# Kernel tuning notes

Hardware: AMD Instinct MI355X
Metric: run time of the kernel (lower is better)

## Reference

```python
import jax, jax.numpy as jnp
import numpy as np

NUM_HEADS = 8


def setup_inputs() -> dict:
    key = jax.random.key(0)
    ks = jax.random.split(key, 9)
    B, S, E = 16, 2048, 768
    s = 0.02
    return {
        "features": jax.random.normal(ks[0], (B, S, E), jnp.float32),
        "in_proj_w": jax.random.normal(ks[1], (3 * E, E), jnp.float32) * s,
        "in_proj_b": jnp.zeros((3 * E,), jnp.float32),
        "out_proj_w": jax.random.normal(ks[2], (E, E), jnp.float32) * s,
        "out_proj_b": jnp.zeros((E,), jnp.float32),
        "w1": jax.random.normal(ks[3], (384, E), jnp.float32) * s,
        "b1": jnp.zeros((384,), jnp.float32),
        "w2": jax.random.normal(ks[4], (1, 384), jnp.float32) * s,
        "b2": jnp.zeros((1,), jnp.float32),
    }


def reference(features, in_proj_w, in_proj_b, out_proj_w, out_proj_b, w1, b1, w2, b2):
    # torch nn.MultiheadAttention default batch_first=False: dim 0 is the
    # attended sequence axis (length B here), dim 1 is the MHA batch (S).
    B, S, E = features.shape
    H = NUM_HEADS
    Dh = E // H
    qkv = features @ in_proj_w.T + in_proj_b          # (B, S, 3E)
    q, k, v = jnp.split(qkv, 3, axis=-1)
    q = q.reshape(B, S, H, Dh)
    k = k.reshape(B, S, H, Dh)
    v = v.reshape(B, S, H, Dh)
    scale = 1.0 / jnp.sqrt(jnp.asarray(Dh, features.dtype))
    # attention over axis-0 positions (l, m in 0..B-1), per (s, h)
    scores = jnp.einsum('lshd,mshd->shlm', q * scale, k)
    attn = jax.nn.softmax(scores, axis=-1)
    ctx = jnp.einsum('shlm,mshd->lshd', attn, v).reshape(B, S, E)
    attn_out = ctx @ out_proj_w.T + out_proj_b        # (B, S, E)
    # batched 2-layer MLP (replaces the Python per-row loop)
    h = jax.nn.relu(attn_out @ w1.T + b1)             # (B, S, 384)
    prob = h @ w2.T + b2                              # (B, S, 1)
    contacts = jnp.broadcast_to(prob, (B, S, S))      # contacts[:, i, :] = prob[:, i]
    return contacts
```

## Files before the change

kernel.cpp:

```cpp
#include <hip/hip_runtime.h>

typedef unsigned short u16;
typedef __attribute__((ext_vector_type(8))) __bf16 bf16x8;
typedef __attribute__((ext_vector_type(4))) float floatx4;

#define B_DIM  16
#define S_DIM  2048
#define E_DIM  768
#define HEADS  8
#define DHEAD  96
#define MROWS  32768
#define QKV_LD 2304
#define ATT_ST 392

#define GLDS(gp, lp) __builtin_amdgcn_global_load_lds( \
    (const __attribute__((address_space(1))) void*)(gp), \
    (__attribute__((address_space(3))) void*)(lp), 16, 0, 0)

__device__ __forceinline__ u16 f2b(float f) {
    unsigned u = __float_as_uint(f);
    u += 0x7fffu + ((u >> 16) & 1u);
    return (u16)(u >> 16);
}
__device__ __forceinline__ float blo(unsigned u) { return __uint_as_float(u << 16); }
__device__ __forceinline__ float bhi(unsigned u) { return __uint_as_float(u & 0xffff0000u); }

__device__ __forceinline__ void axpy8(float* acc, float p, uint4 v) {
    acc[0] += p * blo(v.x); acc[1] += p * bhi(v.x);
    acc[2] += p * blo(v.y); acc[3] += p * bhi(v.y);
    acc[4] += p * blo(v.z); acc[5] += p * bhi(v.z);
    acc[6] += p * blo(v.w); acc[7] += p * bhi(v.w);
}

#define PB0 24576
#define PB1 26304
#define PB2 26592
#define PB3 27168
#define PB4 27552
__global__ __launch_bounds__(256) void prep(const float* __restrict__ features,
                                            const float* __restrict__ in_proj_w,
                                            const float* __restrict__ w1,
                                            const float* __restrict__ out_proj_w,
                                            const float* __restrict__ bo,
                                            const float* __restrict__ b1,
                                            u16* __restrict__ fbf, u16* __restrict__ wib,
                                            u16* __restrict__ w1b, u16* __restrict__ WoT,
                                            float* __restrict__ cbuf) {
    __shared__ float tsh[32][33];
    const int b = blockIdx.x, tid = threadIdx.x;
    if (b < PB2) {
        const float* src; u16* dst; long i;
        if (b < PB0)      { src = features;  dst = fbf; i = (long)b * 256 + tid; }
        else if (b < PB1) { src = in_proj_w; dst = wib; i = (long)(b - PB0) * 256 + tid; }
        else              { src = w1;        dst = w1b; i = (long)(b - PB1) * 256 + tid; }
        float4 f = ((const float4*)src)[i];
        ushort4 r;
        r.x = f2b(f.x); r.y = f2b(f.y); r.z = f2b(f.z); r.w = f2b(f.w);
        ((ushort4*)dst)[i] = r;
    } else if (b < PB3) {
        const int t = b - PB2;
        const int bxT = t % 24, byT = t / 24;
        const int tx = tid & 31, ty = tid >> 5;
        int x = bxT * 32 + tx;
        int y = byT * 32 + ty;
#pragma unroll
        for (int j = 0; j < 4; j++) tsh[ty + j * 8][tx] = out_proj_w[(long)(y + j * 8) * 768 + x];
        __syncthreads();
        x = byT * 32 + tx;
        y = bxT * 32 + ty;
#pragma unroll
        for (int j = 0; j < 4; j++) WoT[(long)(y + j * 8) * 768 + x] = f2b(tsh[tx][ty + j * 8]);
    } else {
        const int n = b - PB3;
        const float* row = w1 + (long)n * 768;
        float s = row[tid] * bo[tid] + row[tid + 256] * bo[tid + 256] + row[tid + 512] * bo[tid + 512];
#pragma unroll
        for (int off = 32; off > 0; off >>= 1) s += __shfl_xor(s, off);
        if ((tid & 63) == 0) tsh[0][tid >> 6] = s;
        __syncthreads();
        if (tid == 0) cbuf[n] = tsh[0][0] + tsh[0][1] + tsh[0][2] + tsh[0][3] + b1[n];
    }
}

__global__ __launch_bounds__(256) void qkv_g_kernel(const u16* __restrict__ A, int lda,
                                                    const u16* __restrict__ W,
                                                    const float* __restrict__ bias,
                                                    u16* __restrict__ Cout, int ldc, int K,
                                                    const u16* __restrict__ gA,
                                                    const u16* __restrict__ gW,
                                                    u16* __restrict__ gC) {
    __shared__ __align__(16) u16 sA[2 * 128 * 32];
    __shared__ __align__(16) u16 sB[2 * 128 * 32];
    __shared__ __align__(16) u16 sC[32 * 132];
    const int tid = threadIdx.x;
    const int bx  = blockIdx.x;
    int bn, bm, lda_, ldc_, K_;
    const u16 *Aa, *Ww; const float* bs; u16* Co; bool perm;
    if (bx < 18) {
        bn = bx % 6; bm = bx / 6;
        Aa = gA; Ww = gW; bs = nullptr; Co = gC;
        lda_ = 768; ldc_ = 768; K_ = 768; perm = false;
    } else {
        const int b2  = bx - 18;
        const int xcd = b2 & 7;
        const int q   = b2 >> 3;
        const int s   = q / 144;
        const int r   = q % 144;
        bn = r >> 3;
        bm = s * 64 + xcd * 8 + (r & 7);
        Aa = A; Ww = W; bs = bias; Co = Cout;
        lda_ = lda; ldc_ = ldc; K_ = K; perm = true;
    }
    const int lane = tid & 63;
    const int wid  = tid >> 6;
    const int wm   = (wid >> 1) * 64;
    const int wn   = (wid & 1) * 64;
    const int ar = tid >> 2;
    const int ac = (tid & 3) * 8;
    const u16* Ap = Aa + (long)(bm * 128 + ar) * lda_ + ac;
    const u16* Wp = Ww + (long)(bn * 128 + ar) * K_ + ac;
    const long a2 = (long)64 * lda_;
    const long w2 = (long)64 * K_;

    floatx4 acc[4][4] = {};
    const int fr = lane & 15;
    const int fq = (lane >> 4) * 8;

    for (int k0 = 0; k0 < K_; k0 += 64) {
#pragma unroll
        for (int h = 0; h < 2; h++) {
            GLDS(Ap + k0 + h * 32,      sA + h * 4096 + tid * 8);
            GLDS(Ap + a2 + k0 + h * 32, sA + h * 4096 + 2048 + tid * 8);
            GLDS(Wp + k0 + h * 32,      sB + h * 4096 + tid * 8);
            GLDS(Wp + w2 + k0 + h * 32, sB + h * 4096 + 2048 + tid * 8);
        }
        __syncthreads();
#pragma unroll
        for (int h = 0; h < 2; h++) {
            bf16x8 aF[4], bF[4];
#pragma unroll
            for (int i = 0; i < 4; i++) {
                aF[i] = *(const bf16x8*)(sA + h * 4096 + (wm + i * 16 + fr) * 32 + fq);
                bF[i] = *(const bf16x8*)(sB + h * 4096 + (wn + i * 16 + fr) * 32 + fq);
            }
#pragma unroll
            for (int i = 0; i < 4; i++)
#pragma unroll
                for (int j = 0; j < 4; j++)
                    acc[i][j] = __builtin_amdgcn_mfma_f32_16x16x32_bf16(aF[i], bF[j], acc[i][j], 0, 0, 0);
        }
        __syncthreads();
    }

    const int rq = (lane >> 4) * 4;
    float bvj[4];
#pragma unroll
    for (int j = 0; j < 4; j++)
        bvj[j] = bs ? bs[bn * 128 + wn + j * 16 + fr] : 0.f;
#pragma unroll
    for (int p = 0; p < 4; p++) {
        if ((p >> 1) == (wid >> 1)) {
#pragma unroll
            for (int ii = 0; ii < 2; ii++) {
                const int i = (p & 1) * 2 + ii;
#pragma unroll
                for (int j = 0; j < 4; j++) {
                    const int col = wn + j * 16 + fr;
#pragma unroll
                    for (int r = 0; r < 4; r++)
                        sC[(ii * 16 + rq + r) * 132 + col] = f2b(acc[i][j][r] + bvj[j]);
                }
            }
        }
        __syncthreads();
#pragma unroll
        for (int q2 = 0; q2 < 2; q2++) {
            const int lr = (tid >> 4) + q2 * 16;
            const int c  = tid & 15;
            uint4 v = *(const uint4*)(sC + lr * 132 + c * 8);
            const int rl = bm * 128 + p * 32 + lr;
            const long grow = perm ? (long)(((rl & 2047) << 4) | (rl >> 11)) : (long)rl;
            *(uint4*)(Co + grow * ldc_ + bn * 128 + c * 8) = v;
        }
        __syncthreads();
    }
}

__global__ __launch_bounds__(256) void attn_kernel(u16* __restrict__ qkv) {
    __shared__ __align__(16) u16 sQ[16 * ATT_ST], sK[16 * ATT_ST], sV[16 * ATT_ST];
    __shared__ float sS[4][16][16];
    const int tid = threadIdx.x;
    const int bx  = blockIdx.x;
    const int xcd   = bx & 7;
    const int rest  = bx >> 3;
    const int hh    = rest & 1;
    const int inner = (rest >> 1) & 63;
    const int outer = rest >> 7;
    const int s = (outer << 9) | (xcd << 6) | inner;
    const u16* base = qkv + (long)s * 16 * QKV_LD + hh * 384;

#pragma unroll
    for (int it = 0; it < 9; it++) {
        const int i = it * 256 + tid;
        const int t = i / 768, rem = i % 768, l = rem / 48, c = rem % 48;
        const u16* src = base + (long)l * QKV_LD + t * E_DIM + c * 8;
        u16* dst = (t == 0 ? sQ : t == 1 ? sK : sV) + l * ATT_ST + c * 8;
        *(uint4*)dst = *(const uint4*)src;
    }
    __syncthreads();

    const int lane = tid & 63;
    const int w    = tid >> 6;
    const int fr   = lane & 15;
    const int fq   = (lane >> 4) * 8;
    floatx4 acc = {};
    const u16* qrow = sQ + fr * ATT_ST + w * DHEAD + fq;
    const u16* krow = sK + fr * ATT_ST + w * DHEAD + fq;
#pragma unroll
    for (int st = 0; st < 3; st++) {
        bf16x8 qa = *(const bf16x8*)(qrow + st * 32);
        bf16x8 kb = *(const bf16x8*)(krow + st * 32);
        acc = __builtin_amdgcn_mfma_f32_16x16x32_bf16(qa, kb, acc, 0, 0, 0);
    }
    const int rq = (lane >> 4) * 4;
#pragma unroll
    for (int r = 0; r < 4; r++) {
        float sc = acc[r] * 0.10206207261596577f;
        float mx = sc;
#pragma unroll
        for (int off = 8; off > 0; off >>= 1) mx = fmaxf(mx, __shfl_xor(mx, off));
        float e = __expf(sc - mx);
        float sum = e;
#pragma unroll
        for (int off = 8; off > 0; off >>= 1) sum += __shfl_xor(sum, off);
        sS[w][rq + r][fr] = e / sum;
    }
    __syncthreads();

#pragma unroll
    for (int j = 0; j < 3; j++) {
        const int task = j * 256 + tid;
        const int h = task / 192, rem = task % 192, ll = rem / 12, c = rem % 12;
        float a[8] = {};
#pragma unroll
        for (int mm = 0; mm < 16; mm++) {
            const float p = sS[h][ll][mm];
            uint4 vw = *(const uint4*)(sV + mm * ATT_ST + h * DHEAD + c * 8);
            axpy8(a, p, vw);
        }
        ushort4 o0, o1;
        o0.x = f2b(a[0]); o0.y = f2b(a[1]); o0.z = f2b(a[2]); o0.w = f2b(a[3]);
        o1.x = f2b(a[4]); o1.y = f2b(a[5]); o1.z = f2b(a[6]); o1.w = f2b(a[7]);
        u16* dst = qkv + ((long)s * 16 + ll) * QKV_LD + (hh * 4 + h) * DHEAD + c * 8;
        *(ushort4*)dst = o0;
        *(ushort4*)(dst + 4) = o1;
    }
}

__global__ __launch_bounds__(256) void mlp_gemm(const u16* __restrict__ A, int lda,
                                                const u16* __restrict__ G,
                                                const float* __restrict__ cbias,
                                                const float* __restrict__ w2,
                                                float* __restrict__ part) {
    __shared__ __align__(16) u16 sA[2 * 128 * 32];
    __shared__ __align__(16) u16 sB[2 * 128 * 32];
    __shared__ float rowsum[128];
    const int tid = threadIdx.x;
    const int bx  = blockIdx.x;
    const int xcd = bx & 7;
    const int q   = bx >> 3;
    const int bn  = q % 3;
    const int t   = q / 3;
    const int bm  = ((t >> 3) << 6) | (xcd << 3) | (t & 7);
    if (tid < 128) rowsum[tid] = 0.f;
    const int lane = tid & 63;
    const int wid  = tid >> 6;
    const int wm   = (wid >> 1) * 64;
    const int wn   = (wid & 1) * 64;
    const int ar = tid >> 2;
    const int ac = (tid & 3) * 8;
    const u16* Ap = A + (long)(bm * 128 + ar) * lda + ac;
    const u16* Wp = G + (long)(bn * 128 + ar) * 768 + ac;
    const long a2 = (long)64 * lda;
    const long w2s = (long)64 * 768;
    const int fr = lane & 15;
    const int fq = (lane >> 4) * 8;
    const int rq = (lane >> 4) * 4;

    floatx4 acc[4][4] = {};
    for (int k0 = 0; k0 < 768; k0 += 64) {
#pragma unroll
        for (int h = 0; h < 2; h++) {
            GLDS(Ap + k0 + h * 32,       sA + h * 4096 + tid * 8);
            GLDS(Ap + a2 + k0 + h * 32,  sA + h * 4096 + 2048 + tid * 8);
            GLDS(Wp + k0 + h * 32,       sB + h * 4096 + tid * 8);
            GLDS(Wp + w2s + k0 + h * 32, sB + h * 4096 + 2048 + tid * 8);
        }
        __syncthreads();
#pragma unroll
        for (int h = 0; h < 2; h++) {
            bf16x8 aF[4], bF[4];
#pragma unroll
            for (int i = 0; i < 4; i++) {
                aF[i] = *(const bf16x8*)(sA + h * 4096 + (wm + i * 16 + fr) * 32 + fq);
                bF[i] = *(const bf16x8*)(sB + h * 4096 + (wn + i * 16 + fr) * 32 + fq);
            }
#pragma unroll
            for (int i = 0; i < 4; i++)
#pragma unroll
                for (int j = 0; j < 4; j++)
                    acc[i][j] = __builtin_amdgcn_mfma_f32_16x16x32_bf16(aF[i], bF[j], acc[i][j], 0, 0, 0);
        }
        __syncthreads();
    }
    float partl[4][4] = {};
#pragma unroll
    for (int j = 0; j < 4; j++) {
        const int col = bn * 128 + wn + j * 16 + fr;
        const float cv = cbias[col];
        const float wv = w2[col];
#pragma unroll
        for (int i = 0; i < 4; i++)
#pragma unroll
            for (int r = 0; r < 4; r++)
                partl[i][r] += fmaxf(acc[i][j][r] + cv, 0.f) * wv;
    }
#pragma unroll
    for (int i = 0; i < 4; i++)
#pragma unroll
        for (int r = 0; r < 4; r++) {
            float v = partl[i][r];
#pragma unroll
            for (int off = 8; off > 0; off >>= 1) v += __shfl_xor(v, off);
            if (fr == 0) atomicAdd(&rowsum[wm + i * 16 + rq + r], v);
        }
    __syncthreads();
    if (tid < 128) part[(long)bn * MROWS + bm * 128 + tid] = rowsum[tid];
}

__global__ __launch_bounds__(256) void bcast_kernel(const float* __restrict__ part,
                                                    const float* __restrict__ b2,
                                                    float* __restrict__ out) {
    const int tid = threadIdx.x;
    const long s  = blockIdx.x;
    const float b2v = b2[0];
#pragma unroll
    for (int l = 0; l < 16; l++) {
        const long p = s * 16 + l;
        const float pv = part[p] + part[MROWS + p] + part[2 * MROWS + p] + b2v;
        floatx4 v4 = {pv, pv, pv, pv};
        floatx4* dst = (floatx4*)(out + ((long)l * S_DIM + s) * S_DIM);
        __builtin_nontemporal_store(v4, dst + tid);
        __builtin_nontemporal_store(v4, dst + tid + 256);
    }
}

extern "C" void kernel_launch(void* const* d_in, const int* in_sizes, int n_in,
                              void* d_out, int out_size, void* d_ws, size_t ws_size,
                              hipStream_t stream) {
    const float* features   = (const float*)d_in[0];
    const float* in_proj_b  = (const float*)d_in[2];
    const float* out_proj_b = (const float*)d_in[4];
    const float* b1 = (const float*)d_in[6];
    const float* w2 = (const float*)d_in[7];
    const float* b2 = (const float*)d_in[8];
    float* out = (float*)d_out;

    char* p = (char*)d_ws;
    u16* fbf = (u16*)p; p += (size_t)MROWS * E_DIM * 2;
    u16* wib = (u16*)p; p += (size_t)QKV_LD * E_DIM * 2;
    u16* w1b = (u16*)p; p += (size_t)384 * E_DIM * 2;
    u16* WoT = (u16*)p; p += (size_t)E_DIM * E_DIM * 2;
    u16* Gbf = (u16*)p; p += (size_t)384 * E_DIM * 2;
    float* cbuf  = (float*)p; p += 384 * 4;
    float* partb = (float*)p; p += (size_t)3 * MROWS * 4;
    p = (char*)(((size_t)p + 255) & ~(size_t)255);
    u16* qkv = (u16*)p; p += (size_t)MROWS * QKV_LD * 2;
    u16* ctx = qkv;

    prep<<<PB4, 256, 0, stream>>>(features, (const float*)d_in[1], (const float*)d_in[5],
                                  (const float*)d_in[3], out_proj_b, b1,
                                  fbf, wib, w1b, WoT, cbuf);
    qkv_g_kernel<<<4626, 256, 0, stream>>>(fbf, E_DIM, wib, in_proj_b, qkv, QKV_LD, E_DIM,
                                           w1b, WoT, Gbf);
    attn_kernel<<<S_DIM * 2, 256, 0, stream>>>(qkv);
    mlp_gemm<<<768, 256, 0, stream>>>(ctx, QKV_LD, Gbf, cbuf, w2, partb);
    bcast_kernel<<<S_DIM, 256, 0, stream>>>(partb, b2, out);
}
```

Measured before the change: 585.1 us.

## Rewrite QKV GEMM with 256x256 tiles, swizzled LDS and double-buffered async loads

Replaces the 128x128-tile QKV projection GEMM with a 512-thread kernel that computes 256x256 tiles. It uses XOR-swizzled LDS, double-buffered global-to-LDS loads issued ahead of the MFMA phases, and s_setprio scheduling around the MFMA blocks. The change aims to raise arithmetic intensity and hide load latency, at the cost of 128KB of LDS per block and more registers. It also remaps the XCD-aware block-to-tile mapping in the attention and MLP kernels to suit the new layout.

```diff
diff --git a/kernel.cpp b/kernel.cpp
--- a/kernel.cpp
+++ b/kernel.cpp
@@ -12,6 +12,7 @@
 #define MROWS  32768
 #define QKV_LD 2304
 #define ATT_ST 392
+#define NT     12
 
 #define GLDS(gp, lp) __builtin_amdgcn_global_load_lds( \
     (const __attribute__((address_space(1))) void*)(gp), \
@@ -30,6 +31,10 @@
     acc[2] += p * blo(v.y); acc[3] += p * bhi(v.y);
     acc[4] += p * blo(v.z); acc[5] += p * bhi(v.z);
     acc[6] += p * blo(v.w); acc[7] += p * bhi(v.w);
+}
+
+__device__ __forceinline__ bf16x8 ldsw(const u16* half_base, int rowh, int cb) {
+    return *(const bf16x8*)((const char*)half_base + rowh * 128 + (cb ^ ((rowh & 7) << 4)));
 }
 
 #define PB0 24576
@@ -82,108 +87,158 @@
     }
 }
 
-__global__ __launch_bounds__(256) void qkv_g_kernel(const u16* __restrict__ A, int lda,
-                                                    const u16* __restrict__ W,
-                                                    const float* __restrict__ bias,
-                                                    u16* __restrict__ Cout, int ldc, int K,
-                                                    const u16* __restrict__ gA,
-                                                    const u16* __restrict__ gW,
-                                                    u16* __restrict__ gC) {
-    __shared__ __align__(16) u16 sA[2 * 128 * 32];
-    __shared__ __align__(16) u16 sB[2 * 128 * 32];
-    __shared__ __align__(16) u16 sC[32 * 132];
+__global__ __launch_bounds__(512, 2) void qkv256(const u16* __restrict__ A,
+                                                 const u16* __restrict__ W,
+                                                 const float* __restrict__ bias,
+                                                 u16* __restrict__ Cout,
+                                                 const u16* __restrict__ gA,
+                                                 const u16* __restrict__ gW,
+                                                 u16* __restrict__ gC) {
+    __shared__ __align__(16) u16 lds[2 * 32768];
     const int tid = threadIdx.x;
     const int bx  = blockIdx.x;
-    int bn, bm, lda_, ldc_, K_;
-    const u16 *Aa, *Ww; const float* bs; u16* Co; bool perm;
-    if (bx < 18) {
-        bn = bx % 6; bm = bx / 6;
-        Aa = gA; Ww = gW; bs = nullptr; Co = gC;
-        lda_ = 768; ldc_ = 768; K_ = 768; perm = false;
+    int bm, bn, ldc, Mvalid; const u16 *Aa, *Ww; const float* bs; u16* Co; bool perm;
+    if (bx < 1152) {
+        const int xcd = bx & 7;
+        const int q   = bx >> 3;
+        bn = q % 9;
+        bm = (q / 9) * 8 + xcd;
+        Aa = A; Ww = W; bs = bias; Co = Cout; ldc = QKV_LD; perm = true; Mvalid = 1 << 30;
     } else {
-        const int b2  = bx - 18;
-        const int xcd = b2 & 7;
-        const int q   = b2 >> 3;
-        const int s   = q / 144;
-        const int r   = q % 144;
-        bn = r >> 3;
-        bm = s * 64 + xcd * 8 + (r & 7);
-        Aa = A; Ww = W; bs = bias; Co = Cout;
-        lda_ = lda; ldc_ = ldc; K_ = K; perm = true;
-    }
-    const int lane = tid & 63;
-    const int wid  = tid >> 6;
-    const int wm   = (wid >> 1) * 64;
-    const int wn   = (wid & 1) * 64;
-    const int ar = tid >> 2;
-    const int ac = (tid & 3) * 8;
-    const u16* Ap = Aa + (long)(bm * 128 + ar) * lda_ + ac;
-    const u16* Wp = Ww + (long)(bn * 128 + ar) * K_ + ac;
-    const long a2 = (long)64 * lda_;
-    const long w2 = (long)64 * K_;
-
-    floatx4 acc[4][4] = {};
-    const int fr = lane & 15;
-    const int fq = (lane >> 4) * 8;
-
-    for (int k0 = 0; k0 < K_; k0 += 64) {
-#pragma unroll
-        for (int h = 0; h < 2; h++) {
-            GLDS(Ap + k0 + h * 32,      sA + h * 4096 + tid * 8);
-            GLDS(Ap + a2 + k0 + h * 32, sA + h * 4096 + 2048 + tid * 8);
-            GLDS(Wp + k0 + h * 32,      sB + h * 4096 + tid * 8);
-            GLDS(Wp + w2 + k0 + h * 32, sB + h * 4096 + 2048 + tid * 8);
-        }
-        __syncthreads();
-#pragma unroll
-        for (int h = 0; h < 2; h++) {
-            bf16x8 aF[4], bF[4];
-#pragma unroll
-            for (int i = 0; i < 4; i++) {
-                aF[i] = *(const bf16x8*)(sA + h * 4096 + (wm + i * 16 + fr) * 32 + fq);
-                bF[i] = *(const bf16x8*)(sB + h * 4096 + (wn + i * 16 + fr) * 32 + fq);
+        const int g = bx - 1152;
+        bn = g % 3; bm = g / 3;
+        Aa = gA; Ww = gW; bs = nullptr; Co = gC; ldc = 768; perm = false; Mvalid = 384;
+    }
+    const int r0 = tid >> 3,        r1 = (tid + 512) >> 3;
+    const int q0 = (tid & 7) ^ (r0 & 7), q1 = ((tid + 512) & 7) ^ (r1 & 7);
+    const u16* pA0 = Aa + (long)(bm * 256 + r0) * 768 + q0 * 8;
+    const u16* pA1 = Aa + (long)(bm * 256 + r1) * 768 + q1 * 8;
+    const u16* pB0 = Ww + (long)(bn * 256 + r0) * 768 + q0 * 8;
+    const u16* pB1 = Ww + (long)(bn * 256 + r1) * 768 + q1 * 8;
+    u16* dA0 = lds + tid * 8;
+    u16* dA1 = lds + 4096 + tid * 8;
+    u16* dB0 = lds + 16384 + tid * 8;
+    u16* dB1 = lds + 16384 + 4096 + tid * 8;
+
+#define IS_A(h, p, t) do { \
+    GLDS(pA0 + (h) * 98304 + (t) * 64, dA0 + (p) * 32768 + (h) * 8192); \
+    GLDS(pA1 + (h) * 98304 + (t) * 64, dA1 + (p) * 32768 + (h) * 8192); } while (0)
+#define IS_B(h, p, t) do { \
+    GLDS(pB0 + (h) * 98304 + (t) * 64, dB0 + (p) * 32768 + (h) * 8192); \
+    GLDS(pB1 + (h) * 98304 + (t) * 64, dB1 + (p) * 32768 + (h) * 8192); } while (0)
+#define MFMA_PRE() do { \
+    __builtin_amdgcn_s_barrier(); \
+    asm volatile("s_waitcnt lgkmcnt(0)" ::: "memory"); \
+    __builtin_amdgcn_sched_barrier(0); \
+    __builtin_amdgcn_s_setprio(1); } while (0)
+#define MFMA_POST() do { \
+    __builtin_amdgcn_s_setprio(0); \
+    __builtin_amdgcn_s_barrier(); } while (0)
+
+    const int lane = tid & 63, wid = tid >> 6;
+    const int wr = wid >> 2, wc = wid & 3;
+    const int fr = lane & 15, fg = lane >> 4;
+    const int fq2 = fg * 16;
+    const int wb  = (wc & 1) * 64;
+    const u16* bufA_base = lds + wr * 8192;
+    const u16* bufB_base = lds + 16384 + (wc >> 1) * 8192;
+
+    IS_A(0, 0, 0); IS_A(1, 0, 0); IS_B(0, 0, 0); IS_B(1, 0, 0);
+    IS_A(0, 1, 1); IS_A(1, 1, 1);
+    asm volatile("s_waitcnt vmcnt(4)" ::: "memory");
+    __builtin_amdgcn_s_barrier();
+
+    floatx4 acc[8][4] = {};
+#pragma unroll 2
+    for (int t = 0; t < NT; ++t) {
+        const int p = t & 1, pn = p ^ 1;
+        const u16* bA = bufA_base + p * 32768;
+        const u16* bB = bufB_base + p * 32768;
+        bf16x8 aF[4], bF[4];
+#pragma unroll
+        for (int i = 0; i < 4; ++i) aF[i] = ldsw(bA, i * 16 + fr, fq2);
+#pragma unroll
+        for (int j = 0; j < 4; ++j) bF[j] = ldsw(bB, wb + j * 16 + fr, fq2);
+        if (t + 1 < NT) IS_B(0, pn, t + 1);
+        MFMA_PRE();
+#pragma unroll
+        for (int i = 0; i < 4; ++i)
+#pragma unroll
+            for (int j = 0; j < 4; ++j)
+                acc[i][j] = __builtin_amdgcn_mfma_f32_16x16x32_bf16(aF[i], bF[j], acc[i][j], 0, 0, 0);
+        MFMA_POST();
+#pragma unroll
+        for (int i = 0; i < 4; ++i) aF[i] = ldsw(bA, (i + 4) * 16 + fr, fq2);
+        if (t + 1 < NT) IS_B(1, pn, t + 1);
+        MFMA_PRE();
+#pragma unroll
+        for (int i = 0; i < 4; ++i)
+#pragma unroll
+            for (int j = 0; j < 4; ++j)
+                acc[i + 4][j] = __builtin_amdgcn_mfma_f32_16x16x32_bf16(aF[i], bF[j], acc[i + 4][j], 0, 0, 0);
+        MFMA_POST();
+#pragma unroll
+        for (int i = 0; i < 4; ++i) aF[i] = ldsw(bA, i * 16 + fr, 64 + fq2);
+#pragma unroll
+        for (int j = 0; j < 4; ++j) bF[j] = ldsw(bB, wb + j * 16 + fr, 64 + fq2);
+        MFMA_PRE();
+#pragma unroll
+        for (int i = 0; i < 4; ++i)
+#pragma unroll
+            for (int j = 0; j < 4; ++j)
+                acc[i][j] = __builtin_amdgcn_mfma_f32_16x16x32_bf16(aF[i], bF[j], acc[i][j], 0, 0, 0);
+        MFMA_POST();
+#pragma unroll
+        for (int i = 0; i < 4; ++i) aF[i] = ldsw(bA, (i + 4) * 16 + fr, 64 + fq2);
+        MFMA_PRE();
+#pragma unroll
+        for (int i = 0; i < 4; ++i)
+#pragma unroll
+            for (int j = 0; j < 4; ++j)
+                acc[i + 4][j] = __builtin_amdgcn_mfma_f32_16x16x32_bf16(aF[i], bF[j], acc[i + 4][j], 0, 0, 0);
+        MFMA_POST();
+        if (t + 2 < NT) {
+            IS_A(0, p, t + 2); IS_A(1, p, t + 2);
+            asm volatile("s_waitcnt vmcnt(4)" ::: "memory");
+            __builtin_amdgcn_s_barrier();
+        } else if (t + 1 < NT) {
+            asm volatile("s_waitcnt vmcnt(0)" ::: "memory");
+            __builtin_amdgcn_s_barrier();
+        }
+    }
+
+    const int rq = fg * 4;
+    float bvj[4];
+#pragma unroll
+    for (int j = 0; j < 4; ++j) bvj[j] = bs ? bs[bn * 256 + wc * 64 + j * 16 + fr] : 0.f;
+    u16* strip = lds + wid * 2048;
+    const int sr = lane >> 3, sc = lane & 7;
+#pragma unroll
+    for (int pass = 0; pass < 4; ++pass) {
+#pragma unroll
+        for (int ii = 0; ii < 2; ++ii) {
+            const int i = pass * 2 + ii;
+#pragma unroll
+            for (int j = 0; j < 4; ++j)
+#pragma unroll
+                for (int r = 0; r < 4; ++r)
+                    strip[(ii * 16 + rq + r) * 64 + j * 16 + fr] = f2b(acc[i][j][r] + bvj[j]);
+        }
+#pragma unroll
+        for (int it = 0; it < 4; ++it) {
+            const int lr = it * 8 + sr;
+            uint4 v = *(const uint4*)(strip + lr * 64 + sc * 8);
+            const int rl = bm * 256 + wr * 128 + pass * 32 + lr;
+            if (rl < Mvalid) {
+                const long grow = perm ? (long)(((rl & 2047) << 4) | (rl >> 11)) : (long)rl;
+                *(uint4*)(Co + grow * ldc + bn * 256 + wc * 64 + sc * 8) = v;
             }
-#pragma unroll
-            for (int i = 0; i < 4; i++)
-#pragma unroll
-                for (int j = 0; j < 4; j++)
-                    acc[i][j] = __builtin_amdgcn_mfma_f32_16x16x32_bf16(aF[i], bF[j], acc[i][j], 0, 0, 0);
-        }
-        __syncthreads();
-    }
-
-    const int rq = (lane >> 4) * 4;
-    float bvj[4];
-#pragma unroll
-    for (int j = 0; j < 4; j++)
-        bvj[j] = bs ? bs[bn * 128 + wn + j * 16 + fr] : 0.f;
-#pragma unroll
-    for (int p = 0; p < 4; p++) {
-        if ((p >> 1) == (wid >> 1)) {
-#pragma unroll
-            for (int ii = 0; ii < 2; ii++) {
-                const int i = (p & 1) * 2 + ii;
-#pragma unroll
-                for (int j = 0; j < 4; j++) {
-                    const int col = wn + j * 16 + fr;
-#pragma unroll
-                    for (int r = 0; r < 4; r++)
-                        sC[(ii * 16 + rq + r) * 132 + col] = f2b(acc[i][j][r] + bvj[j]);
-                }
-            }
-        }
-        __syncthreads();
-#pragma unroll
-        for (int q2 = 0; q2 < 2; q2++) {
-            const int lr = (tid >> 4) + q2 * 16;
-            const int c  = tid & 15;
-            uint4 v = *(const uint4*)(sC + lr * 132 + c * 8);
-            const int rl = bm * 128 + p * 32 + lr;
-            const long grow = perm ? (long)(((rl & 2047) << 4) | (rl >> 11)) : (long)rl;
-            *(uint4*)(Co + grow * ldc_ + bn * 128 + c * 8) = v;
-        }
-        __syncthreads();
-    }
+        }
+    }
+#undef IS_A
+#undef IS_B
+#undef MFMA_PRE
+#undef MFMA_POST
 }
 
 __global__ __launch_bounds__(256) void attn_kernel(u16* __restrict__ qkv) {
@@ -192,11 +247,9 @@
     const int tid = threadIdx.x;
     const int bx  = blockIdx.x;
     const int xcd   = bx & 7;
-    const int rest  = bx >> 3;
-    const int hh    = rest & 1;
-    const int inner = (rest >> 1) & 63;
-    const int outer = rest >> 7;
-    const int s = (outer << 9) | (xcd << 6) | inner;
+    const int hh    = (bx >> 3) & 1;
+    const int inner = bx >> 4;
+    const int s = (xcd << 8) | inner;
     const u16* base = qkv + (long)s * 16 * QKV_LD + hh * 384;
 
 #pragma unroll
@@ -271,7 +324,7 @@
     const int q   = bx >> 3;
     const int bn  = q % 3;
     const int t   = q / 3;
-    const int bm  = ((t >> 3) << 6) | (xcd << 3) | (t & 7);
+    const int bm  = (xcd << 5) | t;
     if (tid < 128) rowsum[tid] = 0.f;
     const int lane = tid & 63;
     const int wid  = tid >> 6;
@@ -381,8 +434,7 @@
     prep<<<PB4, 256, 0, stream>>>(features, (const float*)d_in[1], (const float*)d_in[5],
                                   (const float*)d_in[3], out_proj_b, b1,
                                   fbf, wib, w1b, WoT, cbuf);
-    qkv_g_kernel<<<4626, 256, 0, stream>>>(fbf, E_DIM, wib, in_proj_b, qkv, QKV_LD, E_DIM,
-                                           w1b, WoT, Gbf);
+    qkv256<<<1158, 512, 0, stream>>>(fbf, wib, in_proj_b, qkv, w1b, WoT, Gbf);
     attn_kernel<<<S_DIM * 2, 256, 0, stream>>>(qkv);
     mlp_gemm<<<768, 256, 0, stream>>>(ctx, QKV_LD, Gbf, cbuf, w2, partb);
     bcast_kernel<<<S_DIM, 256, 0, stream>>>(partb, b2, out);
```

New measurement: 555.0 us. 1.05x faster.
